# Kernel optimization log

Hardware: AMD Instinct MI355X
Metric: run time of the kernel (lower is better)

Reference implementation:

```python
import jax, jax.numpy as jnp
import numpy as np

B, NUM, LENTH, AUX = 32, 64, 64, 64
SIZE, OUT = 256, 256
IN_G = (LENTH + 1) * 2 + AUX  # 194


def _linear_params(k, fan_in, fan_out):
    # torch nn.Linear default init: U(-1/sqrt(fan_in), 1/sqrt(fan_in))
    s = 1.0 / np.sqrt(fan_in)
    kw, kb = jax.random.split(k)
    W = jax.random.uniform(kw, (fan_in, fan_out), minval=-s, maxval=s, dtype=jnp.float32)
    b = jax.random.uniform(kb, (fan_out,), minval=-s, maxval=s, dtype=jnp.float32)
    return W, b


def setup_inputs() -> dict:
    key = jax.random.key(0)
    ks = jax.random.split(key, 8)
    inp = {"x_aux": jax.random.normal(ks[0], (B, NUM, LENTH + AUX), dtype=jnp.float32)}
    dims = [("g1", IN_G, SIZE), ("g2", SIZE, SIZE), ("g3", SIZE, SIZE), ("g4", SIZE, OUT),
            ("f1", OUT, SIZE), ("f2", SIZE, SIZE), ("f3", SIZE, OUT)]
    for k, (name, fi, fo) in zip(ks[1:], dims):
        W, b = _linear_params(k, fi, fo)
        inp[name + "_w"] = W
        inp[name + "_b"] = b
    return inp


def reference(x_aux, g1_w, g1_b, g2_w, g2_b, g3_w, g3_b, g4_w, g4_b,
              f1_w, f1_b, f2_w, f2_b, f3_w, f3_b):
    bsz = x_aux.shape[0]
    # coord feature = object index i
    coord = jnp.broadcast_to(
        jnp.arange(NUM, dtype=x_aux.dtype)[None, :, None], (bsz, NUM, 1))
    x = jnp.concatenate([x_aux[:, :, :LENTH], coord], axis=-1)      # [B, N, LENTH+1]
    xa = jnp.concatenate([x_aux, coord], axis=-1)                   # [B, N, LENTH+AUX+1]
    # all-pairs broadcast+concat -> [B, N, N, IN_G]
    x_i = jnp.broadcast_to(x[:, None, :, :], (bsz, NUM, NUM, LENTH + 1))
    x_j = jnp.broadcast_to(xa[:, :, None, :], (bsz, NUM, NUM, LENTH + AUX + 1))
    pairs = jnp.concatenate([x_i, x_j], axis=-1)
    # shared g-MLP over every pair
    h = jax.nn.relu(pairs @ g1_w + g1_b)
    h = jax.nn.relu(h @ g2_w + g2_b)
    h = jax.nn.relu(h @ g3_w + g3_b)
    h = jax.nn.relu(h @ g4_w + g4_b)
    # sum-pool over all N*N pairs -> [B, OUT]
    x_g = h.sum(axis=(1, 2))
    # f-MLP (dropout treated as identity / eval mode)
    x_f = jax.nn.relu(x_g @ f1_w + f1_b)
    x_f = jax.nn.relu(x_f @ f2_w + f2_b)
    return x_f @ f3_w + f3_b
```

## Files before the change

### kernel.cpp

```cpp
#include <hip/hip_runtime.h>

#define BATCH 32
#define NOBJ  64
#define PADK  264

typedef _Float16 f16x2 __attribute__((ext_vector_type(2)));
typedef __fp16   h16x2 __attribute__((ext_vector_type(2)));
typedef _Float16 f16x4 __attribute__((ext_vector_type(4)));
typedef _Float16 f16x8 __attribute__((ext_vector_type(8)));
typedef float    f32x4 __attribute__((ext_vector_type(4)));
typedef float    f32x16 __attribute__((ext_vector_type(16)));

#define MFMA32(a, b, c) __builtin_amdgcn_mfma_f32_32x32x16_f16((a), (b), (c), 0, 0, 0)


__global__ __launch_bounds__(256) void prep_all(
    const float* __restrict__ x_aux,
    const float* __restrict__ g1w, const float* __restrict__ g1b,
    const float* __restrict__ g2w, const float* __restrict__ g3w,
    const float* __restrict__ g4w,
    _Float16* __restrict__ wtf, float* __restrict__ xg,
    float* __restrict__ cib, float* __restrict__ h0j) {
  __shared__ __align__(16) _Float16 tile[256][33];
  const int blk = blockIdx.x;
  const int t = threadIdx.x;

  if (blk < 32) {
    xg[blk * 256 + t] = 0.0f;
    const int l = blk >> 3;
    if (l == 0) return;
    const int nt = blk & 7;
    const float* src = (l == 1) ? g2w : (l == 2) ? g3w : g4w;

    const int nn = t & 31, kb = t >> 5;
#pragma unroll 4
    for (int pass = 0; pass < 32; ++pass) {
      int kp = pass * 8 + kb;
      tile[kp][nn] = (_Float16)src[(size_t)kp * 256 + nt * 32 + nn];
    }
    __syncthreads();

    const int lane = t & 63;
    const int nfrag = lane & 31;
    const int kbase = (lane >> 5) * 8;
    _Float16* dst = wtf + ((size_t)(l * 8 + nt) * 16) * 512;
#pragma unroll
    for (int q = 0; q < 4; ++q) {
      int kk = (t >> 6) + 4 * q;
      f16x8 fr;
#pragma unroll
      for (int j = 0; j < 8; ++j)
        fr[j] = tile[kk * 16 + kbase + j][nfrag];
      *(f16x8*)(dst + (size_t)kk * 512 + lane * 8) = fr;
    }
  } else if (blk < 544) {
    float* xs = (float*)&tile[0][0];
    const int blkc = blk - 32;
    const int b  = blkc >> 4;
    const int i0 = (blkc & 15) * 4;

#pragma unroll
    for (int u = 0; u < 2; ++u) {
      int idx = u * 256 + t;
      int j = idx >> 7, k = idx & 127;
      xs[j * 128 + k] = x_aux[((size_t)(b * NOBJ + i0 + j)) * 128 + k];
    }
    __syncthreads();

    float c0 = 0.f, c1 = 0.f, c2 = 0.f, c3 = 0.f;
#pragma unroll 2
    for (int k = 0; k < 128; k += 4) {
      f32x4 x0 = *(const f32x4*)&xs[k];
      f32x4 x1 = *(const f32x4*)&xs[128 + k];
      f32x4 x2 = *(const f32x4*)&xs[256 + k];
      f32x4 x3 = *(const f32x4*)&xs[384 + k];
#pragma unroll
      for (int q = 0; q < 4; ++q) {
        float w = g1w[(size_t)(65 + k + q) * 256 + t];
        c0 += x0[q] * w; c1 += x1[q] * w;
        c2 += x2[q] * w; c3 += x3[q] * w;
      }
    }
    float wc = g1w[(size_t)193 * 256 + t];
    float bb = g1b[t];
    c0 += (float)(i0 + 0) * wc + bb;
    c1 += (float)(i0 + 1) * wc + bb;
    c2 += (float)(i0 + 2) * wc + bb;
    c3 += (float)(i0 + 3) * wc + bb;
    cib[((size_t)(b * NOBJ + i0 + 0)) * 256 + t] = c0;
    cib[((size_t)(b * NOBJ + i0 + 1)) * 256 + t] = c1;
    cib[((size_t)(b * NOBJ + i0 + 2)) * 256 + t] = c2;
    cib[((size_t)(b * NOBJ + i0 + 3)) * 256 + t] = c3;
  } else {
    float* xs = (float*)&tile[0][0];
    const int blk2 = blk - 544;
    const int b  = blk2 >> 3;
    const int j0 = (blk2 & 7) * 8;

#pragma unroll
    for (int u = 0; u < 2; ++u) {
      int idx = u * 256 + t;
      int jj = idx >> 6, k = idx & 63;
      xs[jj * 68 + k] = x_aux[((size_t)(b * NOBJ + j0 + jj)) * 128 + k];
    }
    __syncthreads();

    float acc[8] = {};
#pragma unroll 2
    for (int k = 0; k < 64; k += 4) {
      f32x4 xv[8];
#pragma unroll
      for (int jj = 0; jj < 8; ++jj)
        xv[jj] = *(const f32x4*)&xs[jj * 68 + k];
#pragma unroll
      for (int q = 0; q < 4; ++q) {
        float w = g1w[(size_t)(k + q) * 256 + t];
#pragma unroll
        for (int jj = 0; jj < 8; ++jj) acc[jj] += xv[jj][q] * w;
      }
    }
    float wc = g1w[(size_t)64 * 256 + t];
#pragma unroll
    for (int jj = 0; jj < 8; ++jj)
      h0j[((size_t)(b * NOBJ + j0 + jj)) * 256 + t] =
          acc[jj] + (float)(j0 + jj) * wc;
  }
}

template <bool PRELOAD_NEXT>
__device__ __forceinline__ void layer_run(
    const _Float16* __restrict__ bp0, const _Float16* __restrict__ bp1,
    const _Float16* __restrict__ bn0, const _Float16* __restrict__ bn1,
    const _Float16* __restrict__ arow,
    f16x8 (&u0)[4], f16x8 (&u1)[4], f32x16 (&acc)[4]) {
#pragma unroll
  for (int kk = 0; kk < 16; ++kk) {
    f16x8 b0 = u0[kk & 3];
    f16x8 b1 = u1[kk & 3];
    f16x8 a0 = *(const f16x8*)(arow + (size_t)kk * 16);
    f16x8 a1 = *(const f16x8*)(arow + (size_t)32 * PADK + kk * 16);
    acc[0] = MFMA32(a0, b0, acc[0]);
    acc[1] = MFMA32(a0, b1, acc[1]);
    acc[2] = MFMA32(a1, b0, acc[2]);
    acc[3] = MFMA32(a1, b1, acc[3]);
    if (kk < 12) {
      u0[kk & 3] = *(const f16x8*)(bp0 + (size_t)(kk + 4) * 512);
      u1[kk & 3] = *(const f16x8*)(bp1 + (size_t)(kk + 4) * 512);
    } else if (PRELOAD_NEXT) {
      u0[kk & 3] = *(const f16x8*)(bn0 + (size_t)(kk - 12) * 512);
      u1[kk & 3] = *(const f16x8*)(bn1 + (size_t)(kk - 12) * 512);
    }
  }
}

__global__ __launch_bounds__(256, 4) void g_mlp_pool(
    const float* __restrict__ h0j,
    const float* __restrict__ cib,
    const _Float16* __restrict__ wtf,
    const float* __restrict__ g2b, const float* __restrict__ g3b,
    const float* __restrict__ g4b,
    float* __restrict__ xg) {
  __shared__ __align__(16) _Float16 As[64][PADK];

  const int b  = blockIdx.x >> 6;
  const int i0 = blockIdx.x & 63;
  const int t  = threadIdx.x;
  const int lane = t & 63;
  const int wv   = t >> 6;

  const int c31  = lane & 31;
  const int h    = lane >> 5;
  const int n0   = wv * 64;

  const _Float16* L1 = wtf + ((size_t)(8  + 2 * wv) * 16) * 512 + lane * 8;
  const _Float16* L2 = wtf + ((size_t)(16 + 2 * wv) * 16) * 512 + lane * 8;
  const _Float16* L3 = wtf + ((size_t)(24 + 2 * wv) * 16) * 512 + lane * 8;

  f16x8 u0[4], u1[4];
#pragma unroll
  for (int q = 0; q < 4; ++q) {
    u0[q] = *(const f16x8*)(L1 + (size_t)q * 512);
    u1[q] = *(const f16x8*)(L1 + 16 * 512 + (size_t)q * 512);
  }

  {
    const int c = lane * 4;
    const float* hb = h0j + (size_t)(b * NOBJ) * 256 + c;
    f32x4 cv = *(const f32x4*)(cib + (size_t)(b * NOBJ + i0) * 256 + c);
#pragma unroll
    for (int it = 0; it < 16; ++it) {
      int j = it * 4 + wv;
      f32x4 hv = *(const f32x4*)(hb + (size_t)j * 256);
      f16x4 p;
#pragma unroll
      for (int q = 0; q < 4; ++q)
        p[q] = (_Float16)fmaxf(hv[q] + cv[q], 0.f);
      *(f16x4*)&As[j][c] = p;
    }
  }
  __syncthreads();

  const _Float16* arow = &As[c31][h * 8];
  const float bv20 = g2b[n0 + c31], bv21 = g2b[n0 + 32 + c31];
  const float bv30 = g3b[n0 + c31], bv31 = g3b[n0 + 32 + c31];
  const float bv40 = g4b[n0 + c31], bv41 = g4b[n0 + 32 + c31];

  f32x16 acc[4];

#pragma unroll
  for (int x = 0; x < 4; ++x) acc[x] = (f32x16){};
  layer_run<true>(L1, L1 + 16 * 512, L2, L2 + 16 * 512, arow, u0, u1, acc);

  __syncthreads();
#pragma unroll
  for (int m = 0; m < 2; ++m)
#pragma unroll
    for (int g = 0; g < 4; ++g)
#pragma unroll
      for (int r = 0; r < 4; ++r) {
        const int row = m * 32 + g * 8 + h * 4 + r;
        const int reg = g * 4 + r;
        As[row][n0 + c31]      = (_Float16)fmaxf(acc[m * 2][reg] + bv20, 0.f);
        As[row][n0 + 32 + c31] = (_Float16)fmaxf(acc[m * 2 + 1][reg] + bv21, 0.f);
      }
  __syncthreads();

#pragma unroll
  for (int x = 0; x < 4; ++x) acc[x] = (f32x16){};
  layer_run<true>(L2, L2 + 16 * 512, L3, L3 + 16 * 512, arow, u0, u1, acc);

  __syncthreads();
#pragma unroll
  for (int m = 0; m < 2; ++m)
#pragma unroll
    for (int g = 0; g < 4; ++g)
#pragma unroll
      for (int r = 0; r < 4; ++r) {
        const int row = m * 32 + g * 8 + h * 4 + r;
        const int reg = g * 4 + r;
        As[row][n0 + c31]      = (_Float16)fmaxf(acc[m * 2][reg] + bv30, 0.f);
        As[row][n0 + 32 + c31] = (_Float16)fmaxf(acc[m * 2 + 1][reg] + bv31, 0.f);
      }
  __syncthreads();

#pragma unroll
  for (int x = 0; x < 4; ++x) acc[x] = (f32x16){};
  layer_run<false>(L3, L3 + 16 * 512, nullptr, nullptr, arow, u0, u1, acc);

  float s0 = 0.f, s1 = 0.f;
#pragma unroll
  for (int m = 0; m < 2; ++m)
#pragma unroll
    for (int reg = 0; reg < 16; ++reg) {
      s0 += fmaxf(acc[m * 2][reg] + bv40, 0.f);
      s1 += fmaxf(acc[m * 2 + 1][reg] + bv41, 0.f);
    }
  s0 += __shfl_xor(s0, 32, 64);
  s1 += __shfl_xor(s1, 32, 64);
  if (h == 0) {
    atomicAdd(&xg[b * 256 + n0 + c31], s0);
    atomicAdd(&xg[b * 256 + n0 + 32 + c31], s1);
  }
}

__global__ __launch_bounds__(1024) void f_mlp(
    const float* __restrict__ xg,
    const float* __restrict__ f1w, const float* __restrict__ f1b,
    const float* __restrict__ f2w, const float* __restrict__ f2b,
    const float* __restrict__ f3w, const float* __restrict__ f3b,
    float* __restrict__ out) {
  __shared__ float xs[256], ys[256], ps[4][256];
  const int b = blockIdx.x;
  const int t = threadIdx.x;
  const int n = t & 255;
  const int kc = t >> 8;

  if (t < 256) xs[t] = xg[b * 256 + t];
  __syncthreads();

  float p = 0.f;
#pragma unroll 8
  for (int k0 = 0; k0 < 64; ++k0) {
    int k = kc * 64 + k0;
    p += xs[k] * f1w[k * 256 + n];
  }
  ps[kc][n] = p;
  __syncthreads();
  if (t < 256)
    ys[t] = fmaxf(f1b[t] + ps[0][t] + ps[1][t] + ps[2][t] + ps[3][t], 0.f);
  __syncthreads();

  p = 0.f;
#pragma unroll 8
  for (int k0 = 0; k0 < 64; ++k0) {
    int k = kc * 64 + k0;
    p += ys[k] * f2w[k * 256 + n];
  }
  ps[kc][n] = p;
  __syncthreads();
  if (t < 256)
    xs[t] = fmaxf(f2b[t] + ps[0][t] + ps[1][t] + ps[2][t] + ps[3][t], 0.f);
  __syncthreads();

  p = 0.f;
#pragma unroll 8
  for (int k0 = 0; k0 < 64; ++k0) {
    int k = kc * 64 + k0;
    p += xs[k] * f3w[k * 256 + n];
  }
  ps[kc][n] = p;
  __syncthreads();
  if (t < 256)
    out[b * 256 + t] = f3b[t] + ps[0][t] + ps[1][t] + ps[2][t] + ps[3][t];
}

extern "C" void kernel_launch(void* const* d_in, const int* in_sizes, int n_in,
                              void* d_out, int out_size, void* d_ws, size_t ws_size,
                              hipStream_t stream) {
  const float* x_aux = (const float*)d_in[0];
  const float* g1w = (const float*)d_in[1];
  const float* g1b = (const float*)d_in[2];
  const float* g2w = (const float*)d_in[3];
  const float* g2b = (const float*)d_in[4];
  const float* g3w = (const float*)d_in[5];
  const float* g3b = (const float*)d_in[6];
  const float* g4w = (const float*)d_in[7];
  const float* g4b = (const float*)d_in[8];
  const float* f1w = (const float*)d_in[9];
  const float* f1b = (const float*)d_in[10];
  const float* f2w = (const float*)d_in[11];
  const float* f2b = (const float*)d_in[12];
  const float* f3w = (const float*)d_in[13];
  const float* f3b = (const float*)d_in[14];
  float* out = (float*)d_out;

  _Float16* wtf = (_Float16*)d_ws;
  float* xg  = (float*)((char*)d_ws + 512u * 1024u);
  float* cib = (float*)((char*)d_ws + 544u * 1024u);
  float* h0j = (float*)((char*)d_ws + 544u * 1024u + 2048u * 1024u);

  hipLaunchKernelGGL(prep_all, dim3(800), dim3(256), 0, stream,
                     x_aux, g1w, g1b, g2w, g3w, g4w, wtf, xg, cib, h0j);
  hipLaunchKernelGGL(g_mlp_pool, dim3(BATCH * NOBJ), dim3(256), 0, stream,
                     h0j, cib, wtf, g2b, g3b, g4b, xg);
  hipLaunchKernelGGL(f_mlp, dim3(BATCH), dim3(1024), 0, stream,
                     xg, f1w, f1b, f2w, f2b, f3w, f3b, out);
}
```

Before: 154.8 us.

## Double-buffer LDS activations, deepen weight prefetch, raise MFMA wave priority

Activations now ping-pong between two LDS buffers, so each layer's epilogue writes the other buffer and one of the two __syncthreads per layer is dropped. The weight-fragment register prefetch depth grows from 4 to 8 k-steps, and s_setprio raises wave priority around the MFMA loop. In exchange, LDS per block doubles and more registers are used, so launch bounds drop from 4 to 2 blocks per SM. The lower occupancy may reduce latency hiding.

New measurement: 155.7 us. Within noise of the previous version (+0.6%).

```diff
diff --git a/kernel.cpp b/kernel.cpp
--- a/kernel.cpp
+++ b/kernel.cpp
@@ -132,35 +132,53 @@
     const _Float16* __restrict__ bp0, const _Float16* __restrict__ bp1,
     const _Float16* __restrict__ bn0, const _Float16* __restrict__ bn1,
     const _Float16* __restrict__ arow,
-    f16x8 (&u0)[4], f16x8 (&u1)[4], f32x16 (&acc)[4]) {
+    f16x8 (&u0)[8], f16x8 (&u1)[8], f32x16 (&acc)[4]) {
+  __builtin_amdgcn_s_setprio(1);
 #pragma unroll
   for (int kk = 0; kk < 16; ++kk) {
-    f16x8 b0 = u0[kk & 3];
-    f16x8 b1 = u1[kk & 3];
+    f16x8 b0 = u0[kk & 7];
+    f16x8 b1 = u1[kk & 7];
     f16x8 a0 = *(const f16x8*)(arow + (size_t)kk * 16);
     f16x8 a1 = *(const f16x8*)(arow + (size_t)32 * PADK + kk * 16);
     acc[0] = MFMA32(a0, b0, acc[0]);
     acc[1] = MFMA32(a0, b1, acc[1]);
     acc[2] = MFMA32(a1, b0, acc[2]);
     acc[3] = MFMA32(a1, b1, acc[3]);
-    if (kk < 12) {
-      u0[kk & 3] = *(const f16x8*)(bp0 + (size_t)(kk + 4) * 512);
-      u1[kk & 3] = *(const f16x8*)(bp1 + (size_t)(kk + 4) * 512);
-    } else if (PRELOAD_NEXT) {
-      u0[kk & 3] = *(const f16x8*)(bn0 + (size_t)(kk - 12) * 512);
-      u1[kk & 3] = *(const f16x8*)(bn1 + (size_t)(kk - 12) * 512);
-    }
-  }
-}
-
-__global__ __launch_bounds__(256, 4) void g_mlp_pool(
+    if (kk < 8) {
+      u0[kk & 7] = *(const f16x8*)(bp0 + (size_t)(kk + 8) * 512);
+      u1[kk & 7] = *(const f16x8*)(bp1 + (size_t)(kk + 8) * 512);
+    } else if constexpr (PRELOAD_NEXT) {
+      u0[kk & 7] = *(const f16x8*)(bn0 + (size_t)(kk - 8) * 512);
+      u1[kk & 7] = *(const f16x8*)(bn1 + (size_t)(kk - 8) * 512);
+    }
+  }
+  __builtin_amdgcn_s_setprio(0);
+}
+
+__device__ __forceinline__ void epilogue_store(
+    _Float16 (*__restrict__ dst)[PADK], const f32x16 (&acc)[4],
+    float bv0, float bv1, int n0, int c31, int h) {
+#pragma unroll
+  for (int m = 0; m < 2; ++m)
+#pragma unroll
+    for (int g = 0; g < 4; ++g)
+#pragma unroll
+      for (int r = 0; r < 4; ++r) {
+        const int row = m * 32 + g * 8 + h * 4 + r;
+        const int reg = g * 4 + r;
+        dst[row][n0 + c31]      = (_Float16)fmaxf(acc[m * 2][reg] + bv0, 0.f);
+        dst[row][n0 + 32 + c31] = (_Float16)fmaxf(acc[m * 2 + 1][reg] + bv1, 0.f);
+      }
+}
+
+__global__ __launch_bounds__(256, 2) void g_mlp_pool(
     const float* __restrict__ h0j,
     const float* __restrict__ cib,
     const _Float16* __restrict__ wtf,
     const float* __restrict__ g2b, const float* __restrict__ g3b,
     const float* __restrict__ g4b,
     float* __restrict__ xg) {
-  __shared__ __align__(16) _Float16 As[64][PADK];
+  __shared__ __align__(16) _Float16 As[2][64][PADK];
 
   const int b  = blockIdx.x >> 6;
   const int i0 = blockIdx.x & 63;
@@ -176,9 +194,9 @@
   const _Float16* L2 = wtf + ((size_t)(16 + 2 * wv) * 16) * 512 + lane * 8;
   const _Float16* L3 = wtf + ((size_t)(24 + 2 * wv) * 16) * 512 + lane * 8;
 
-  f16x8 u0[4], u1[4];
-#pragma unroll
-  for (int q = 0; q < 4; ++q) {
+  f16x8 u0[8], u1[8];
+#pragma unroll
+  for (int q = 0; q < 8; ++q) {
     u0[q] = *(const f16x8*)(L1 + (size_t)q * 512);
     u1[q] = *(const f16x8*)(L1 + 16 * 512 + (size_t)q * 512);
   }
@@ -195,12 +213,13 @@
 #pragma unroll
       for (int q = 0; q < 4; ++q)
         p[q] = (_Float16)fmaxf(hv[q] + cv[q], 0.f);
-      *(f16x4*)&As[j][c] = p;
-    }
-  }
-  __syncthreads();
-
-  const _Float16* arow = &As[c31][h * 8];
+      *(f16x4*)&As[0][j][c] = p;
+    }
+  }
+  __syncthreads();
+
+  const _Float16* a0 = &As[0][c31][h * 8];
+  const _Float16* a1 = &As[1][c31][h * 8];
   const float bv20 = g2b[n0 + c31], bv21 = g2b[n0 + 32 + c31];
   const float bv30 = g3b[n0 + c31], bv31 = g3b[n0 + 32 + c31];
   const float bv40 = g4b[n0 + c31], bv41 = g4b[n0 + 32 + c31];
@@ -209,43 +228,19 @@
 
 #pragma unroll
   for (int x = 0; x < 4; ++x) acc[x] = (f32x16){};
-  layer_run<true>(L1, L1 + 16 * 512, L2, L2 + 16 * 512, arow, u0, u1, acc);
-
-  __syncthreads();
-#pragma unroll
-  for (int m = 0; m < 2; ++m)
-#pragma unroll
-    for (int g = 0; g < 4; ++g)
-#pragma unroll
-      for (int r = 0; r < 4; ++r) {
-        const int row = m * 32 + g * 8 + h * 4 + r;
-        const int reg = g * 4 + r;
-        As[row][n0 + c31]      = (_Float16)fmaxf(acc[m * 2][reg] + bv20, 0.f);
-        As[row][n0 + 32 + c31] = (_Float16)fmaxf(acc[m * 2 + 1][reg] + bv21, 0.f);
-      }
+  layer_run<true>(L1, L1 + 16 * 512, L2, L2 + 16 * 512, a0, u0, u1, acc);
+  epilogue_store(As[1], acc, bv20, bv21, n0, c31, h);
   __syncthreads();
 
 #pragma unroll
   for (int x = 0; x < 4; ++x) acc[x] = (f32x16){};
-  layer_run<true>(L2, L2 + 16 * 512, L3, L3 + 16 * 512, arow, u0, u1, acc);
-
-  __syncthreads();
-#pragma unroll
-  for (int m = 0; m < 2; ++m)
-#pragma unroll
-    for (int g = 0; g < 4; ++g)
-#pragma unroll
-      for (int r = 0; r < 4; ++r) {
-        const int row = m * 32 + g * 8 + h * 4 + r;
-        const int reg = g * 4 + r;
-        As[row][n0 + c31]      = (_Float16)fmaxf(acc[m * 2][reg] + bv30, 0.f);
-        As[row][n0 + 32 + c31] = (_Float16)fmaxf(acc[m * 2 + 1][reg] + bv31, 0.f);
-      }
+  layer_run<true>(L2, L2 + 16 * 512, L3, L3 + 16 * 512, a1, u0, u1, acc);
+  epilogue_store(As[0], acc, bv30, bv31, n0, c31, h);
   __syncthreads();
 
 #pragma unroll
   for (int x = 0; x < 4; ++x) acc[x] = (f32x16){};
-  layer_run<false>(L3, L3 + 16 * 512, nullptr, nullptr, arow, u0, u1, acc);
+  layer_run<false>(L3, L3 + 16 * 512, nullptr, nullptr, a0, u0, u1, acc);
 
   float s0 = 0.f, s1 = 0.f;
 #pragma unroll
```

## Process two i-rows per block to double M tile and reuse weight fragments

Applied to the files above, without the earlier changes.

Each block of the g-MLP kernel now handles 128 pair rows (two i values) instead of 64, so every weight fragment loaded from global memory feeds twice as many MFMAs. A fragments are double-buffered in registers ahead of use, and the grid is halved. The cost is doubled accumulators and LDS (about 66KB per block), so launch bounds drop to one block per SM hint and occupancy falls, with fewer blocks to spread across CUs.

New measurement: 153.5 us. No clear change (-0.8%).

```diff
diff --git a/kernel.cpp b/kernel.cpp
--- a/kernel.cpp
+++ b/kernel.cpp
@@ -132,38 +132,51 @@
     const _Float16* __restrict__ bp0, const _Float16* __restrict__ bp1,
     const _Float16* __restrict__ bn0, const _Float16* __restrict__ bn1,
     const _Float16* __restrict__ arow,
-    f16x8 (&u0)[4], f16x8 (&u1)[4], f32x16 (&acc)[4]) {
+    f16x8 (&av)[2][4], f16x8 (&u0)[4], f16x8 (&u1)[4],
+    f32x16 (&acc)[8]) {
+#pragma unroll
+  for (int p = 0; p < 2; ++p)
+#pragma unroll
+    for (int m = 0; m < 4; ++m)
+      av[p][m] = *(const f16x8*)(arow + (size_t)m * 32 * PADK + p * 16);
+
 #pragma unroll
   for (int kk = 0; kk < 16; ++kk) {
     f16x8 b0 = u0[kk & 3];
     f16x8 b1 = u1[kk & 3];
-    f16x8 a0 = *(const f16x8*)(arow + (size_t)kk * 16);
-    f16x8 a1 = *(const f16x8*)(arow + (size_t)32 * PADK + kk * 16);
-    acc[0] = MFMA32(a0, b0, acc[0]);
-    acc[1] = MFMA32(a0, b1, acc[1]);
-    acc[2] = MFMA32(a1, b0, acc[2]);
-    acc[3] = MFMA32(a1, b1, acc[3]);
+#pragma unroll
+    for (int m = 0; m < 4; ++m) {
+      f16x8 a = av[kk & 1][m];
+      acc[m * 2]     = MFMA32(a, b0, acc[m * 2]);
+      acc[m * 2 + 1] = MFMA32(a, b1, acc[m * 2 + 1]);
+    }
+    if (kk < 14) {
+#pragma unroll
+      for (int m = 0; m < 4; ++m)
+        av[kk & 1][m] =
+            *(const f16x8*)(arow + (size_t)m * 32 * PADK + (kk + 2) * 16);
+    }
     if (kk < 12) {
       u0[kk & 3] = *(const f16x8*)(bp0 + (size_t)(kk + 4) * 512);
       u1[kk & 3] = *(const f16x8*)(bp1 + (size_t)(kk + 4) * 512);
-    } else if (PRELOAD_NEXT) {
+    } else if constexpr (PRELOAD_NEXT) {
       u0[kk & 3] = *(const f16x8*)(bn0 + (size_t)(kk - 12) * 512);
       u1[kk & 3] = *(const f16x8*)(bn1 + (size_t)(kk - 12) * 512);
     }
   }
 }
 
-__global__ __launch_bounds__(256, 4) void g_mlp_pool(
+__global__ __launch_bounds__(256, 1) void g_mlp_pool(
     const float* __restrict__ h0j,
     const float* __restrict__ cib,
     const _Float16* __restrict__ wtf,
     const float* __restrict__ g2b, const float* __restrict__ g3b,
     const float* __restrict__ g4b,
     float* __restrict__ xg) {
-  __shared__ __align__(16) _Float16 As[64][PADK];
-
-  const int b  = blockIdx.x >> 6;
-  const int i0 = blockIdx.x & 63;
+  __shared__ __align__(16) _Float16 As[128][PADK];
+
+  const int b  = blockIdx.x >> 5;
+  const int i0 = (blockIdx.x & 31) * 2;
   const int t  = threadIdx.x;
   const int lane = t & 63;
   const int wv   = t >> 6;
@@ -186,16 +199,21 @@
   {
     const int c = lane * 4;
     const float* hb = h0j + (size_t)(b * NOBJ) * 256 + c;
-    f32x4 cv = *(const f32x4*)(cib + (size_t)(b * NOBJ + i0) * 256 + c);
+    const float* c0p = cib + (size_t)(b * NOBJ + i0) * 256 + c;
+    f32x4 cv0 = *(const f32x4*)c0p;
+    f32x4 cv1 = *(const f32x4*)(c0p + 256);
 #pragma unroll
     for (int it = 0; it < 16; ++it) {
       int j = it * 4 + wv;
       f32x4 hv = *(const f32x4*)(hb + (size_t)j * 256);
-      f16x4 p;
-#pragma unroll
-      for (int q = 0; q < 4; ++q)
-        p[q] = (_Float16)fmaxf(hv[q] + cv[q], 0.f);
-      *(f16x4*)&As[j][c] = p;
+      f16x4 p0, p1;
+#pragma unroll
+      for (int q = 0; q < 4; ++q) {
+        p0[q] = (_Float16)fmaxf(hv[q] + cv0[q], 0.f);
+        p1[q] = (_Float16)fmaxf(hv[q] + cv1[q], 0.f);
+      }
+      *(f16x4*)&As[j][c]      = p0;
+      *(f16x4*)&As[64 + j][c] = p1;
     }
   }
   __syncthreads();
@@ -205,15 +223,16 @@
   const float bv30 = g3b[n0 + c31], bv31 = g3b[n0 + 32 + c31];
   const float bv40 = g4b[n0 + c31], bv41 = g4b[n0 + 32 + c31];
 
-  f32x16 acc[4];
-
-#pragma unroll
-  for (int x = 0; x < 4; ++x) acc[x] = (f32x16){};
-  layer_run<true>(L1, L1 + 16 * 512, L2, L2 + 16 * 512, arow, u0, u1, acc);
-
-  __syncthreads();
-#pragma unroll
-  for (int m = 0; m < 2; ++m)
+  f16x8 av[2][4];
+  f32x16 acc[8];
+
+#pragma unroll
+  for (int x = 0; x < 8; ++x) acc[x] = (f32x16){};
+  layer_run<true>(L1, L1 + 16 * 512, L2, L2 + 16 * 512, arow, av, u0, u1, acc);
+
+  __syncthreads();
+#pragma unroll
+  for (int m = 0; m < 4; ++m)
 #pragma unroll
     for (int g = 0; g < 4; ++g)
 #pragma unroll
@@ -226,12 +245,12 @@
   __syncthreads();
 
 #pragma unroll
-  for (int x = 0; x < 4; ++x) acc[x] = (f32x16){};
-  layer_run<true>(L2, L2 + 16 * 512, L3, L3 + 16 * 512, arow, u0, u1, acc);
-
-  __syncthreads();
-#pragma unroll
-  for (int m = 0; m < 2; ++m)
+  for (int x = 0; x < 8; ++x) acc[x] = (f32x16){};
+  layer_run<true>(L2, L2 + 16 * 512, L3, L3 + 16 * 512, arow, av, u0, u1, acc);
+
+  __syncthreads();
+#pragma unroll
+  for (int m = 0; m < 4; ++m)
 #pragma unroll
     for (int g = 0; g < 4; ++g)
 #pragma unroll
@@ -244,12 +263,12 @@
   __syncthreads();
 
 #pragma unroll
-  for (int x = 0; x < 4; ++x) acc[x] = (f32x16){};
-  layer_run<false>(L3, L3 + 16 * 512, nullptr, nullptr, arow, u0, u1, acc);
+  for (int x = 0; x < 8; ++x) acc[x] = (f32x16){};
+  layer_run<false>(L3, L3 + 16 * 512, nullptr, nullptr, arow, av, u0, u1, acc);
 
   float s0 = 0.f, s1 = 0.f;
 #pragma unroll
-  for (int m = 0; m < 2; ++m)
+  for (int m = 0; m < 4; ++m)
 #pragma unroll
     for (int reg = 0; reg < 16; ++reg) {
       s0 += fmaxf(acc[m * 2][reg] + bv40, 0.f);
@@ -341,7 +360,7 @@
 
   hipLaunchKernelGGL(prep_all, dim3(800), dim3(256), 0, stream,
                      x_aux, g1w, g1b, g2w, g3w, g4w, wtf, xg, cib, h0j);
-  hipLaunchKernelGGL(g_mlp_pool, dim3(BATCH * NOBJ), dim3(256), 0, stream,
+  hipLaunchKernelGGL(g_mlp_pool, dim3(BATCH * 32), dim3(256), 0, stream,
                      h0j, cib, wtf, g2b, g3b, g4b, xg);
   hipLaunchKernelGGL(f_mlp, dim3(BATCH), dim3(1024), 0, stream,
                      xg, f1w, f1b, f2w, f2b, f3w, f3b, out);
```
